# Kernel tuning notes

Hardware: AMD Instinct MI355X
Metric: run time of the kernel (lower is better)

The kernel has to match this reference:

```python
import jax, jax.numpy as jnp
import numpy as np

B, T, F, H, C = 256, 128, 256, 512, 10


def setup_inputs() -> dict:
    key = jax.random.key(0)
    ks = jax.random.split(key, 11)
    s_in = 1.0 / np.sqrt(H)  # torch RNN init scale ~ U(-1/sqrt(H), 1/sqrt(H)); use scaled normal
    return {
        "x": jax.random.normal(ks[0], (B, T, F), jnp.float32),
        "W_ih0": jax.random.normal(ks[1], (H, F), jnp.float32) * s_in,
        "W_hh0": jax.random.normal(ks[2], (H, H), jnp.float32) * s_in,
        "b_ih0": jax.random.normal(ks[3], (H,), jnp.float32) * s_in,
        "b_hh0": jax.random.normal(ks[4], (H,), jnp.float32) * s_in,
        "W_ih1": jax.random.normal(ks[5], (H, H), jnp.float32) * s_in,
        "W_hh1": jax.random.normal(ks[6], (H, H), jnp.float32) * s_in,
        "b_ih1": jax.random.normal(ks[7], (H,), jnp.float32) * s_in,
        "b_hh1": jax.random.normal(ks[8], (H,), jnp.float32) * s_in,
        "W_fc": jax.random.normal(ks[9], (C, H * T), jnp.float32) * (1.0 / np.sqrt(H * T)),
        "b_fc": jax.random.normal(ks[10], (C,), jnp.float32) * 0.01,
    }


def _rnn_layer(inp, W_ih, W_hh, b_ih, b_hh):
    # inp: [B, T, Fin]. Precompute all input-to-hidden projections in one GEMM.
    proj = jnp.einsum('btf,hf->bth', inp, W_ih) + b_ih + b_hh  # [B, T, H]

    def step(h, p_t):
        h_new = jax.nn.relu(p_t + h @ W_hh.T)  # h_t = relu(x W_ih^T + b_ih + h_{t-1} W_hh^T + b_hh)
        return h_new, h_new

    h0 = jnp.zeros((inp.shape[0], W_hh.shape[0]), inp.dtype)
    _, outs = jax.lax.scan(step, h0, jnp.swapaxes(proj, 0, 1))  # scan over T
    return jnp.swapaxes(outs, 0, 1)  # [B, T, H]


def reference(x, W_ih0, W_hh0, b_ih0, b_hh0, W_ih1, W_hh1, b_ih1, b_hh1, W_fc, b_fc):
    h = _rnn_layer(x, W_ih0, W_hh0, b_ih0, b_hh0)
    h = _rnn_layer(h, W_ih1, W_hh1, b_ih1, b_hh1)
    flat = h.reshape(h.shape[0], -1)  # [B, T*H]
    return flat @ W_fc.T + b_fc  # [B, C]
```

## Files before the change

kernel.cpp:

```cpp
#include <hip/hip_runtime.h>
#include <cstddef>

#define B_ 256
#define T_ 128
#define F_ 256
#define H_ 512
#define C_ 10

#define TEAMS 32
#define TB    8
#define BS    8
#define NS    64

typedef short bf16x8 __attribute__((ext_vector_type(8)));
typedef float f32x4  __attribute__((ext_vector_type(4)));

__device__ __forceinline__ unsigned short f2bf_rn(float f) {
    unsigned u = __builtin_bit_cast(unsigned, f);
    u += 0x7fffu + ((u >> 16) & 1u);
    return (unsigned short)(u >> 16);
}
__device__ __forceinline__ float bf2f(unsigned short s) {
    unsigned u = (unsigned)s << 16;
    return __builtin_bit_cast(float, u);
}

template<int K>
__global__ __launch_bounds__(256, 2) void gemm_bias_kernel(
    const float* __restrict__ A, const float* __restrict__ W,
    const float* __restrict__ b1, const float* __restrict__ b2,
    float* __restrict__ Cout)
{
    __shared__ alignas(16) float As[16][132];
    __shared__ alignas(16) float Ws[16][132];

    const int tid = threadIdx.x;
    const int m0 = blockIdx.x * 128;
    const int n0 = blockIdx.y * 128;
    const int tx = tid & 15;
    const int ty = tid >> 4;

    float acc[8][8];
#pragma unroll
    for (int i = 0; i < 8; i++)
#pragma unroll
        for (int j = 0; j < 8; j++) acc[i][j] = 0.f;

    for (int k0 = 0; k0 < K; k0 += 16) {
#pragma unroll
        for (int i = 0; i < 2; i++) {
            int f = tid + 256 * i;
            int m = f >> 2, k4 = (f & 3) * 4;
            float4 v = *(const float4*)(A + (size_t)(m0 + m) * K + k0 + k4);
            As[k4 + 0][m] = v.x; As[k4 + 1][m] = v.y;
            As[k4 + 2][m] = v.z; As[k4 + 3][m] = v.w;
        }
#pragma unroll
        for (int i = 0; i < 2; i++) {
            int f = tid + 256 * i;
            int n = f >> 2, k4 = (f & 3) * 4;
            float4 v = *(const float4*)(W + (size_t)(n0 + n) * K + k0 + k4);
            Ws[k4 + 0][n] = v.x; Ws[k4 + 1][n] = v.y;
            Ws[k4 + 2][n] = v.z; Ws[k4 + 3][n] = v.w;
        }
        __syncthreads();

#pragma unroll
        for (int kk = 0; kk < 16; kk++) {
            float4 a0 = *(const float4*)&As[kk][ty * 8];
            float4 a1 = *(const float4*)&As[kk][ty * 8 + 4];
            float4 w0 = *(const float4*)&Ws[kk][tx * 8];
            float4 w1 = *(const float4*)&Ws[kk][tx * 8 + 4];
            float a[8] = {a0.x, a0.y, a0.z, a0.w, a1.x, a1.y, a1.z, a1.w};
            float w[8] = {w0.x, w0.y, w0.z, w0.w, w1.x, w1.y, w1.z, w1.w};
#pragma unroll
            for (int i = 0; i < 8; i++)
#pragma unroll
                for (int j = 0; j < 8; j++)
                    acc[i][j] = fmaf(a[i], w[j], acc[i][j]);
        }
        __syncthreads();
    }

    float bias[8];
#pragma unroll
    for (int j = 0; j < 8; j++) {
        int n = n0 + tx * 8 + j;
        bias[j] = b1[n] + b2[n];
    }
#pragma unroll
    for (int i = 0; i < 8; i++) {
        int m = m0 + ty * 8 + i;
        float4 v0 = {acc[i][0] + bias[0], acc[i][1] + bias[1],
                     acc[i][2] + bias[2], acc[i][3] + bias[3]};
        float4 v1 = {acc[i][4] + bias[4], acc[i][5] + bias[5],
                     acc[i][6] + bias[6], acc[i][7] + bias[7]};
        *(float4*)(Cout + (size_t)m * H_ + n0 + tx * 8)     = v0;
        *(float4*)(Cout + (size_t)m * H_ + n0 + tx * 8 + 4) = v1;
    }
}

__device__ __forceinline__ void load_wfrag(
    const float* __restrict__ W, int wrow, int khalf, int koct,
    bf16x8* bhi, bf16x8* blo)
{
#pragma unroll
    for (int ks = 0; ks < 8; ks++) {
        const float* wp = W + (size_t)wrow * H_ + khalf + ks * 32 + koct;
        const unsigned long long* q = (const unsigned long long*)wp;
        float f[8];
#pragma unroll
        for (int j = 0; j < 4; j++) {
            union { unsigned long long q; float f[2]; } u;
            u.q = __hip_atomic_load(q + j, __ATOMIC_RELAXED,
                                    __HIP_MEMORY_SCOPE_AGENT);
            f[2 * j] = u.f[0]; f[2 * j + 1] = u.f[1];
        }
#pragma unroll
        for (int j = 0; j < 8; j++) {
            unsigned short hi = f2bf_rn(f[j]);
            unsigned short lo = f2bf_rn(f[j] - bf2f(hi));
            bhi[ks][j] = (short)hi;
            blo[ks][j] = (short)lo;
        }
    }
}

__global__ __launch_bounds__(512, 2) void fused_scan_kernel(
    float* __restrict__ ws0, float* __restrict__ ws1,
    const float* __restrict__ Whh0, const float* __restrict__ Wih1,
    const float* __restrict__ Whh1,
    const float* __restrict__ bih1, const float* __restrict__ bhh1,
    unsigned int* __restrict__ bar)
{
    __shared__ alignas(16) unsigned short hs0_hi[BS * H_];
    __shared__ alignas(16) unsigned short hs0_lo[BS * H_];
    __shared__ alignas(16) unsigned short hs1_hi[BS * H_];
    __shared__ alignas(16) unsigned short hs1_lo[BS * H_];
    __shared__ alignas(16) float red0[8][8][17];
    __shared__ alignas(16) float red1[8][8][17];

    const int tid   = threadIdx.x;
    const int team  = blockIdx.x & 31;
    const int mem   = blockIdx.x >> 5;
    const int b0    = team * BS;
    const int n0    = mem * NS;
    const int lane  = tid & 63;
    const int wv    = tid >> 6;
    const int ct    = wv >> 1;
    const int khalf = (wv & 1) << 8;

    unsigned int* cnt = bar + team * 16;

    const int wrow = n0 + (ct << 4) + (lane & 15);
    const int koct = (lane >> 4) << 3;
    bf16x8 w0hi[8], w0lo[8], wihi[8], wilo[8], w1hi[8], w1lo[8];
    load_wfrag(Whh0, wrow, khalf, koct, w0hi, w0lo);
    load_wfrag(Wih1, wrow, khalf, koct, wihi, wilo);
    load_wfrag(Whh1, wrow, khalf, koct, w1hi, w1lo);

    const int bb = tid >> 6;
    const int cc = tid & 63;
    float* p0 = ws0 + ((size_t)(b0 + bb) * T_) * H_ + n0 + cc;
    float* p1 = ws1 + ((size_t)(b0 + bb) * T_) * H_ + n0 + cc;
    float projv = *p0;
    const float bias1v = bih1[n0 + cc] + bhh1[n0 + cc];

    const int qw    = tid & 255;
    const int rhalf = (tid >> 8) * 4;

    const int arow  = lane & 7;
    const int rbase = arow << 10;
    const int kxor  = arow << 4;
    const int klane = (lane >> 4) << 4;

    for (int r = 0; r <= T_; r++) {
        if (r == 0) {
            ((float4*)hs0_hi)[tid] = float4{0.f, 0.f, 0.f, 0.f};
            ((float4*)hs0_lo)[tid] = float4{0.f, 0.f, 0.f, 0.f};
        } else {
            const float* sp = ws0 + ((size_t)b0 * T_ + (r - 1)) * H_;
#pragma unroll
            for (int i = 0; i < 4; i++) {
                const int b = rhalf + i;
                unsigned long long v = __hip_atomic_load(
                    (const unsigned long long*)(sp + (size_t)b * T_ * H_) + qw,
                    __ATOMIC_RELAXED, __HIP_MEMORY_SCOPE_AGENT);
                union { unsigned long long q; float f[2]; } u; u.q = v;
                unsigned short h0 = f2bf_rn(u.f[0]);
                unsigned short h1 = f2bf_rn(u.f[1]);
                unsigned short l0 = f2bf_rn(u.f[0] - bf2f(h0));
                unsigned short l1 = f2bf_rn(u.f[1] - bf2f(h1));
                const int addr = ((b << 10) | (qw << 2)) ^ (b << 4);
                *(unsigned int*)((char*)hs0_hi + addr) =
                    (unsigned int)h0 | ((unsigned int)h1 << 16);
                *(unsigned int*)((char*)hs0_lo + addr) =
                    (unsigned int)l0 | ((unsigned int)l1 << 16);
            }
        }
        if (r <= 1) {
            ((float4*)hs1_hi)[tid] = float4{0.f, 0.f, 0.f, 0.f};
            ((float4*)hs1_lo)[tid] = float4{0.f, 0.f, 0.f, 0.f};
        } else {
            const float* sp = ws1 + ((size_t)b0 * T_ + (r - 2)) * H_;
#pragma unroll
            for (int i = 0; i < 4; i++) {
                const int b = rhalf + i;
                unsigned long long v = __hip_atomic_load(
                    (const unsigned long long*)(sp + (size_t)b * T_ * H_) + qw,
                    __ATOMIC_RELAXED, __HIP_MEMORY_SCOPE_AGENT);
                union { unsigned long long q; float f[2]; } u; u.q = v;
                unsigned short h0 = f2bf_rn(u.f[0]);
                unsigned short h1 = f2bf_rn(u.f[1]);
                unsigned short l0 = f2bf_rn(u.f[0] - bf2f(h0));
                unsigned short l1 = f2bf_rn(u.f[1] - bf2f(h1));
                const int addr = ((b << 10) | (qw << 2)) ^ (b << 4);
                *(unsigned int*)((char*)hs1_hi + addr) =
                    (unsigned int)h0 | ((unsigned int)h1 << 16);
                *(unsigned int*)((char*)hs1_lo + addr) =
                    (unsigned int)l0 | ((unsigned int)l1 << 16);
            }
        }
        __syncthreads();

        f32x4 a0x = {0.f,0.f,0.f,0.f}, a0y = {0.f,0.f,0.f,0.f};
        f32x4 a1x = {0.f,0.f,0.f,0.f}, a1y = {0.f,0.f,0.f,0.f};
#pragma unroll
        for (int ks = 0; ks < 8; ks++) {
            const int kbyte = (khalf << 1) + ks * 64 + klane;
            const int addr  = rbase | (kbyte ^ kxor);
            bf16x8 h0hi = *(const bf16x8*)((const char*)hs0_hi + addr);
            bf16x8 h0lo = *(const bf16x8*)((const char*)hs0_lo + addr);
            bf16x8 h1hi = *(const bf16x8*)((const char*)hs1_hi + addr);
            bf16x8 h1lo = *(const bf16x8*)((const char*)hs1_lo + addr);
            if ((ks & 1) == 0) {
                a0x = __builtin_amdgcn_mfma_f32_16x16x32_bf16(h0hi, w0hi[ks], a0x, 0, 0, 0);
                a0x = __builtin_amdgcn_mfma_f32_16x16x32_bf16(h0hi, w0lo[ks], a0x, 0, 0, 0);
                a0x = __builtin_amdgcn_mfma_f32_16x16x32_bf16(h0lo, w0hi[ks], a0x, 0, 0, 0);
                a1x = __builtin_amdgcn_mfma_f32_16x16x32_bf16(h0hi, wihi[ks], a1x, 0, 0, 0);
                a1x = __builtin_amdgcn_mfma_f32_16x16x32_bf16(h0hi, wilo[ks], a1x, 0, 0, 0);
                a1x = __builtin_amdgcn_mfma_f32_16x16x32_bf16(h0lo, wihi[ks], a1x, 0, 0, 0);
                a1x = __builtin_amdgcn_mfma_f32_16x16x32_bf16(h1hi, w1hi[ks], a1x, 0, 0, 0);
                a1x = __builtin_amdgcn_mfma_f32_16x16x32_bf16(h1hi, w1lo[ks], a1x, 0, 0, 0);
                a1x = __builtin_amdgcn_mfma_f32_16x16x32_bf16(h1lo, w1hi[ks], a1x, 0, 0, 0);
            } else {
                a0y = __builtin_amdgcn_mfma_f32_16x16x32_bf16(h0hi, w0hi[ks], a0y, 0, 0, 0);
                a0y = __builtin_amdgcn_mfma_f32_16x16x32_bf16(h0hi, w0lo[ks], a0y, 0, 0, 0);
                a0y = __builtin_amdgcn_mfma_f32_16x16x32_bf16(h0lo, w0hi[ks], a0y, 0, 0, 0);
                a1y = __builtin_amdgcn_mfma_f32_16x16x32_bf16(h0hi, wihi[ks], a1y, 0, 0, 0);
                a1y = __builtin_amdgcn_mfma_f32_16x16x32_bf16(h0hi, wilo[ks], a1y, 0, 0, 0);
                a1y = __builtin_amdgcn_mfma_f32_16x16x32_bf16(h0lo, wihi[ks], a1y, 0, 0, 0);
                a1y = __builtin_amdgcn_mfma_f32_16x16x32_bf16(h1hi, w1hi[ks], a1y, 0, 0, 0);
                a1y = __builtin_amdgcn_mfma_f32_16x16x32_bf16(h1hi, w1lo[ks], a1y, 0, 0, 0);
                a1y = __builtin_amdgcn_mfma_f32_16x16x32_bf16(h1lo, w1hi[ks], a1y, 0, 0, 0);
            }
        }

        if (lane < 32) {
            const int rrow = (lane >> 4) << 2;
            const int col  = lane & 15;
#pragma unroll
            for (int q = 0; q < 4; q++) {
                red0[wv][rrow + q][col] = a0x[q] + a0y[q];
                red1[wv][rrow + q][col] = a1x[q] + a1y[q];
            }
        }
        __syncthreads();

        {
            const int wv0 = (cc >> 4) << 1;
            const int ci  = cc & 15;
            if (r < T_) {
                float s0 = red0[wv0][bb][ci] + red0[wv0 + 1][bb][ci];
                float h  = fmaxf(s0 + projv, 0.f);
                __hip_atomic_store(p0 + (size_t)r * H_, h,
                                   __ATOMIC_RELAXED, __HIP_MEMORY_SCOPE_AGENT);
            }
            if (r >= 1) {
                float s1 = red1[wv0][bb][ci] + red1[wv0 + 1][bb][ci];
                float h  = fmaxf(s1 + bias1v, 0.f);
                __hip_atomic_store(p1 + (size_t)(r - 1) * H_, h,
                                   __ATOMIC_RELAXED, __HIP_MEMORY_SCOPE_AGENT);
            }
        }

        if (r < T_) {
            __syncthreads();
            if (tid == 0)
                __hip_atomic_fetch_add(cnt, 1u,
                                       __ATOMIC_RELAXED, __HIP_MEMORY_SCOPE_AGENT);
            float nextproj = 0.f;
            if (r + 1 < T_)
                nextproj = p0[(size_t)(r + 1) * H_];
            if (tid == 0) {
                const unsigned target = (unsigned)TB * (unsigned)(r + 1);
                while (__hip_atomic_load(cnt, __ATOMIC_RELAXED,
                                         __HIP_MEMORY_SCOPE_AGENT) < target) {
                    __builtin_amdgcn_s_sleep(1);
                }
            }
            __syncthreads();
            projv = nextproj;
        }
    }
}

__global__ __launch_bounds__(256) void fc_kernel(
    const float* __restrict__ Hl, const float* __restrict__ Wfc,
    const float* __restrict__ bfc, float* __restrict__ out)
{
    const int b = blockIdx.x;
    const int tid = threadIdx.x;
    const float* hb = Hl + (size_t)b * (T_ * H_);

    float acc[C_];
#pragma unroll
    for (int c = 0; c < C_; c++) acc[c] = 0.f;

    for (int i = tid * 4; i < T_ * H_; i += 256 * 4) {
        float4 hv = *(const float4*)(hb + i);
#pragma unroll
        for (int c = 0; c < C_; c++) {
            float4 wv = *(const float4*)(Wfc + (size_t)c * (T_ * H_) + i);
            acc[c] = fmaf(hv.x, wv.x, fmaf(hv.y, wv.y,
                     fmaf(hv.z, wv.z, fmaf(hv.w, wv.w, acc[c]))));
        }
    }

    __shared__ float red[4][C_];
#pragma unroll
    for (int c = 0; c < C_; c++) {
        float v = acc[c];
#pragma unroll
        for (int off = 32; off >= 1; off >>= 1) v += __shfl_xor(v, off, 64);
        if ((tid & 63) == 0) red[tid >> 6][c] = v;
    }
    __syncthreads();
    if (tid < C_) {
        float v = red[0][tid] + red[1][tid] + red[2][tid] + red[3][tid] + bfc[tid];
        out[(size_t)b * C_ + tid] = v;
    }
}

extern "C" void kernel_launch(void* const* d_in, const int* in_sizes, int n_in,
                              void* d_out, int out_size, void* d_ws, size_t ws_size,
                              hipStream_t stream)
{
    (void)in_sizes; (void)n_in; (void)out_size; (void)ws_size;

    const float* x    = (const float*)d_in[0];
    const float* Wih0 = (const float*)d_in[1];
    const float* Whh0 = (const float*)d_in[2];
    const float* bih0 = (const float*)d_in[3];
    const float* bhh0 = (const float*)d_in[4];
    const float* Wih1 = (const float*)d_in[5];
    const float* Whh1 = (const float*)d_in[6];
    const float* bih1 = (const float*)d_in[7];
    const float* bhh1 = (const float*)d_in[8];
    const float* Wfc  = (const float*)d_in[9];
    const float* bfc  = (const float*)d_in[10];
    float* out = (float*)d_out;

    float* ws0 = (float*)d_ws;
    float* ws1 = ws0 + (size_t)B_ * T_ * H_;
    unsigned int* bar = (unsigned int*)d_out;

    hipMemsetAsync(bar, 0, TEAMS * 16 * sizeof(unsigned int), stream);

    dim3 gproj(B_ * T_ / 128, H_ / 128);

    gemm_bias_kernel<F_><<<gproj, 256, 0, stream>>>(x, Wih0, bih0, bhh0, ws0);
    fused_scan_kernel<<<TEAMS * TB, 512, 0, stream>>>(
        ws0, ws1, Whh0, Wih1, Whh1, bih1, bhh1, bar);
    fc_kernel<<<B_, 256, 0, stream>>>(ws1, Wfc, bfc, out);
}
```

Baseline: 847.2 us.

## Exchange packed bf16 hi/lo hidden states through small double-buffered rings

Hidden states shared between blocks each step now go through two small double-buffered global ring buffers (2×B×H each). They are stored already split into bf16 hi/lo pairs, so readers no longer do the split conversion on every load. Layer-1 outputs are written to the full-history workspace off the critical path, and the FC kernel reconstructs the floats from the packed pairs. This cuts per-step conversion work and keeps the inter-block exchange in a small, cache-friendly footprint, at the cost of a two-slot buffer reuse that relies on the existing per-step barrier. The FC input now carries only hi+lo bf16 precision, about 16 mantissa bits.

Result: slower. 901.7 us (+6.4%).

```diff
diff --git a/kernel.cpp b/kernel.cpp
--- a/kernel.cpp
+++ b/kernel.cpp
@@ -15,6 +15,9 @@
 typedef short bf16x8 __attribute__((ext_vector_type(8)));
 typedef float f32x4  __attribute__((ext_vector_type(4)));
 
+__device__ __attribute__((aligned(16))) unsigned g_ring0[2 * B_ * H_];
+__device__ __attribute__((aligned(16))) unsigned g_ring1[2 * B_ * H_];
+
 __device__ __forceinline__ unsigned short f2bf_rn(float f) {
     unsigned u = __builtin_bit_cast(unsigned, f);
     u += 0x7fffu + ((u >> 16) & 1u);
@@ -23,6 +26,11 @@
 __device__ __forceinline__ float bf2f(unsigned short s) {
     unsigned u = (unsigned)s << 16;
     return __builtin_bit_cast(float, u);
+}
+__device__ __forceinline__ unsigned packh(float h) {
+    unsigned short hi = f2bf_rn(h);
+    unsigned short lo = f2bf_rn(h - bf2f(hi));
+    return (unsigned)hi | ((unsigned)lo << 16);
 }
 
 template<int K>
@@ -127,7 +135,7 @@
 }
 
 __global__ __launch_bounds__(512, 2) void fused_scan_kernel(
-    float* __restrict__ ws0, float* __restrict__ ws1,
+    const float* __restrict__ proj0, unsigned* __restrict__ ws1p,
     const float* __restrict__ Whh0, const float* __restrict__ Wih1,
     const float* __restrict__ Whh1,
     const float* __restrict__ bih1, const float* __restrict__ bhh1,
@@ -161,10 +169,12 @@
 
     const int bb = tid >> 6;
     const int cc = tid & 63;
-    float* p0 = ws0 + ((size_t)(b0 + bb) * T_) * H_ + n0 + cc;
-    float* p1 = ws1 + ((size_t)(b0 + bb) * T_) * H_ + n0 + cc;
+    const float* p0 = proj0 + ((size_t)(b0 + bb) * T_) * H_ + n0 + cc;
     float projv = *p0;
     const float bias1v = bih1[n0 + cc] + bhh1[n0 + cc];
+    unsigned* r0out = g_ring0 + (size_t)(b0 + bb) * H_ + n0 + cc;
+    unsigned* r1out = g_ring1 + (size_t)(b0 + bb) * H_ + n0 + cc;
+    unsigned* w1out = ws1p + ((size_t)(b0 + bb) * T_) * H_ + n0 + cc;
 
     const int qw    = tid & 255;
     const int rhalf = (tid >> 8) * 4;
@@ -179,46 +189,40 @@
             ((float4*)hs0_hi)[tid] = float4{0.f, 0.f, 0.f, 0.f};
             ((float4*)hs0_lo)[tid] = float4{0.f, 0.f, 0.f, 0.f};
         } else {
-            const float* sp = ws0 + ((size_t)b0 * T_ + (r - 1)) * H_;
+            const unsigned* sp =
+                g_ring0 + ((size_t)((r - 1) & 1) * B_ + b0) * H_;
 #pragma unroll
             for (int i = 0; i < 4; i++) {
                 const int b = rhalf + i;
                 unsigned long long v = __hip_atomic_load(
-                    (const unsigned long long*)(sp + (size_t)b * T_ * H_) + qw,
+                    (const unsigned long long*)(sp + (size_t)b * H_) + qw,
                     __ATOMIC_RELAXED, __HIP_MEMORY_SCOPE_AGENT);
-                union { unsigned long long q; float f[2]; } u; u.q = v;
-                unsigned short h0 = f2bf_rn(u.f[0]);
-                unsigned short h1 = f2bf_rn(u.f[1]);
-                unsigned short l0 = f2bf_rn(u.f[0] - bf2f(h0));
-                unsigned short l1 = f2bf_rn(u.f[1] - bf2f(h1));
+                const unsigned u0 = (unsigned)v, u1 = (unsigned)(v >> 32);
                 const int addr = ((b << 10) | (qw << 2)) ^ (b << 4);
-                *(unsigned int*)((char*)hs0_hi + addr) =
-                    (unsigned int)h0 | ((unsigned int)h1 << 16);
-                *(unsigned int*)((char*)hs0_lo + addr) =
-                    (unsigned int)l0 | ((unsigned int)l1 << 16);
+                *(unsigned*)((char*)hs0_hi + addr) =
+                    (u0 & 0xFFFFu) | (u1 << 16);
+                *(unsigned*)((char*)hs0_lo + addr) =
+                    (u0 >> 16) | (u1 & 0xFFFF0000u);
             }
         }
         if (r <= 1) {
             ((float4*)hs1_hi)[tid] = float4{0.f, 0.f, 0.f, 0.f};
             ((float4*)hs1_lo)[tid] = float4{0.f, 0.f, 0.f, 0.f};
         } else {
-            const float* sp = ws1 + ((size_t)b0 * T_ + (r - 2)) * H_;
+            const unsigned* sp =
+                g_ring1 + ((size_t)(r & 1) * B_ + b0) * H_;
 #pragma unroll
             for (int i = 0; i < 4; i++) {
                 const int b = rhalf + i;
                 unsigned long long v = __hip_atomic_load(
-                    (const unsigned long long*)(sp + (size_t)b * T_ * H_) + qw,
+                    (const unsigned long long*)(sp + (size_t)b * H_) + qw,
                     __ATOMIC_RELAXED, __HIP_MEMORY_SCOPE_AGENT);
-                union { unsigned long long q; float f[2]; } u; u.q = v;
-                unsigned short h0 = f2bf_rn(u.f[0]);
-                unsigned short h1 = f2bf_rn(u.f[1]);
-                unsigned short l0 = f2bf_rn(u.f[0] - bf2f(h0));
-                unsigned short l1 = f2bf_rn(u.f[1] - bf2f(h1));
+                const unsigned u0 = (unsigned)v, u1 = (unsigned)(v >> 32);
                 const int addr = ((b << 10) | (qw << 2)) ^ (b << 4);
-                *(unsigned int*)((char*)hs1_hi + addr) =
-                    (unsigned int)h0 | ((unsigned int)h1 << 16);
-                *(unsigned int*)((char*)hs1_lo + addr) =
-                    (unsigned int)l0 | ((unsigned int)l1 << 16);
+                *(unsigned*)((char*)hs1_hi + addr) =
+                    (u0 & 0xFFFFu) | (u1 << 16);
+                *(unsigned*)((char*)hs1_lo + addr) =
+                    (u0 >> 16) | (u1 & 0xFFFF0000u);
             }
         }
         __syncthreads();
@@ -267,19 +271,23 @@
         }
         __syncthreads();
 
+        unsigned pk1 = 0;
         {
             const int wv0 = (cc >> 4) << 1;
             const int ci  = cc & 15;
             if (r < T_) {
                 float s0 = red0[wv0][bb][ci] + red0[wv0 + 1][bb][ci];
                 float h  = fmaxf(s0 + projv, 0.f);
-                __hip_atomic_store(p0 + (size_t)r * H_, h,
+                __hip_atomic_store(r0out + (size_t)(r & 1) * B_ * H_,
+                                   packh(h),
                                    __ATOMIC_RELAXED, __HIP_MEMORY_SCOPE_AGENT);
             }
             if (r >= 1) {
                 float s1 = red1[wv0][bb][ci] + red1[wv0 + 1][bb][ci];
                 float h  = fmaxf(s1 + bias1v, 0.f);
-                __hip_atomic_store(p1 + (size_t)(r - 1) * H_, h,
+                pk1 = packh(h);
+                __hip_atomic_store(r1out + (size_t)((r - 1) & 1) * B_ * H_,
+                                   pk1,
                                    __ATOMIC_RELAXED, __HIP_MEMORY_SCOPE_AGENT);
             }
         }
@@ -289,6 +297,8 @@
             if (tid == 0)
                 __hip_atomic_fetch_add(cnt, 1u,
                                        __ATOMIC_RELAXED, __HIP_MEMORY_SCOPE_AGENT);
+            if (r >= 1)
+                w1out[(size_t)(r - 1) * H_] = pk1;
             float nextproj = 0.f;
             if (r + 1 < T_)
                 nextproj = p0[(size_t)(r + 1) * H_];
@@ -301,29 +311,39 @@
             }
             __syncthreads();
             projv = nextproj;
+        } else {
+            w1out[(size_t)(T_ - 1) * H_] = pk1;
         }
     }
 }
 
 __global__ __launch_bounds__(256) void fc_kernel(
-    const float* __restrict__ Hl, const float* __restrict__ Wfc,
+    const unsigned* __restrict__ Hl, const float* __restrict__ Wfc,
     const float* __restrict__ bfc, float* __restrict__ out)
 {
     const int b = blockIdx.x;
     const int tid = threadIdx.x;
-    const float* hb = Hl + (size_t)b * (T_ * H_);
+    const unsigned* hb = Hl + (size_t)b * (T_ * H_);
 
     float acc[C_];
 #pragma unroll
     for (int c = 0; c < C_; c++) acc[c] = 0.f;
 
     for (int i = tid * 4; i < T_ * H_; i += 256 * 4) {
-        float4 hv = *(const float4*)(hb + i);
+        uint4 hv = *(const uint4*)(hb + i);
+        float h0 = bf2f((unsigned short)(hv.x & 0xFFFFu)) +
+                   bf2f((unsigned short)(hv.x >> 16));
+        float h1 = bf2f((unsigned short)(hv.y & 0xFFFFu)) +
+                   bf2f((unsigned short)(hv.y >> 16));
+        float h2 = bf2f((unsigned short)(hv.z & 0xFFFFu)) +
+                   bf2f((unsigned short)(hv.z >> 16));
+        float h3 = bf2f((unsigned short)(hv.w & 0xFFFFu)) +
+                   bf2f((unsigned short)(hv.w >> 16));
 #pragma unroll
         for (int c = 0; c < C_; c++) {
             float4 wv = *(const float4*)(Wfc + (size_t)c * (T_ * H_) + i);
-            acc[c] = fmaf(hv.x, wv.x, fmaf(hv.y, wv.y,
-                     fmaf(hv.z, wv.z, fmaf(hv.w, wv.w, acc[c]))));
+            acc[c] = fmaf(h0, wv.x, fmaf(h1, wv.y,
+                     fmaf(h2, wv.z, fmaf(h3, wv.w, acc[c]))));
         }
     }
 
@@ -361,16 +381,16 @@
     const float* bfc  = (const float*)d_in[10];
     float* out = (float*)d_out;
 
-    float* ws0 = (float*)d_ws;
-    float* ws1 = ws0 + (size_t)B_ * T_ * H_;
+    float*    proj0 = (float*)d_ws;
+    unsigned* ws1p  = (unsigned*)(proj0 + (size_t)B_ * T_ * H_);
     unsigned int* bar = (unsigned int*)d_out;
 
     hipMemsetAsync(bar, 0, TEAMS * 16 * sizeof(unsigned int), stream);
 
     dim3 gproj(B_ * T_ / 128, H_ / 128);
 
-    gemm_bias_kernel<F_><<<gproj, 256, 0, stream>>>(x, Wih0, bih0, bhh0, ws0);
+    gemm_bias_kernel<F_><<<gproj, 256, 0, stream>>>(x, Wih0, bih0, bhh0, proj0);
     fused_scan_kernel<<<TEAMS * TB, 512, 0, stream>>>(
-        ws0, ws1, Whh0, Wih1, Whh1, bih1, bhh1, bar);
-    fc_kernel<<<B_, 256, 0, stream>>>(ws1, Wfc, bfc, out);
-}
+        proj0, ws1p, Whh0, Wih1, Whh1, bih1, bhh1, bar);
+    fc_kernel<<<B_, 256, 0, stream>>>(ws1p, Wfc, bfc, out);
+}
```
